# Optimization experiments

Measured on AMD Instinct MI355X. Metric: run time of the kernel, lower is better.

Reference implementation:

```python
import jax, jax.numpy as jnp
import numpy as np

N, E, B, D, R, L = 60000, 600000, 512, 128, 30, 3
CUT_LOW, CUT_HIGH = 0.0, 10.0
N_ATOM_TYPES = 100


def _sp(x, beta, threshold):
    # torch.nn.Softplus(beta, threshold): x if beta*x > threshold else log1p(exp(beta*x))/beta
    bx = beta * x
    return jnp.where(bx > threshold, x, jnp.log1p(jnp.exp(jnp.minimum(bx, threshold))) / beta)


def setup_inputs() -> dict:
    key = jax.random.key(0)
    ks = jax.random.split(key, 16)

    def lin(k, fi, fo):
        k1, k2 = jax.random.split(k)
        W = jax.random.normal(k1, (fi, fo), jnp.float32) * (fi ** -0.5)
        b = jax.random.normal(k2, (fo,), jnp.float32) * 0.01
        return W, b

    def lin_stack(k, fi, fo, n):
        Ws, bs = zip(*[lin(kk, fi, fo) for kk in jax.random.split(k, n)])
        return jnp.stack(Ws), jnp.stack(bs)

    inp = {}
    inp['atom_type'] = jax.random.randint(ks[0], (N,), 0, N_ATOM_TYPES)
    inp['src'] = jax.random.randint(ks[1], (E,), 0, N)
    inp['dst'] = jax.random.randint(ks[2], (E,), 0, N)
    inp['graph_ids'] = jnp.sort(jax.random.randint(ks[3], (N,), 0, B))
    inp['dist'] = jax.random.uniform(ks[4], (E,), jnp.float32) * CUT_HIGH
    inp['node_emb'] = jax.random.normal(ks[5], (N_ATOM_TYPES, D), jnp.float32) * 0.1
    inp['W_n1'], inp['b_n1'] = lin_stack(ks[6], D, D, L)
    inp['W_c1'], inp['b_c1'] = lin_stack(ks[7], R, D, L)
    inp['W_c2'], inp['b_c2'] = lin_stack(ks[8], D, D, L)
    inp['W_c3'], inp['b_c3'] = lin_stack(ks[9], D, D, L)
    inp['W_n2'], inp['b_n2'] = lin_stack(ks[10], D, D, L)
    inp['W_n3'], inp['b_n3'] = lin_stack(ks[11], D, D, L)
    inp['W_r1'], inp['b_r1'] = lin(ks[12], D * (L + 1), 64)
    inp['W_r2'], inp['b_r2'] = lin(ks[13], 64, 1)
    return inp


def reference(atom_type, src, dst, graph_ids, dist, node_emb,
              W_n1, b_n1, W_c1, b_c1, W_c2, b_c2, W_c3, b_c3,
              W_n2, b_n2, W_n3, b_n3, W_r1, b_r1, W_r2, b_r2):
    # RBF expansion of edge distances: exp(-(d - mu_k)^2 / gap)  -> [E, R]
    centers = jnp.linspace(CUT_LOW, CUT_HIGH, R).astype(dist.dtype)
    gap = centers[1] - centers[0]
    rbf = jnp.exp(-((dist[:, None] - centers) ** 2) / gap)

    h = node_emb[atom_type]  # node embedding lookup [N, D]
    hs = [h]
    for i in range(L):  # MultiLevelInteraction layers (fixed small count)
        h_new = hs[-1] @ W_n1[i] + b_n1[i]                       # node_layer1 [N, D]
        # VEConv edge MLP on rbf (linear1 -> softplus(0.5,14) -> linear2 -> linear3)
        e = _sp(rbf @ W_c1[i] + b_c1[i], 0.5, 14.0) @ W_c2[i] + b_c2[i]
        e = e @ W_c3[i] + b_c3[i]                                 # [E, D]
        # sum_e(h_new[src]*e) + sum_e(e) fused into one scatter-sum over dst
        msg = (h_new[src] + 1.0) * e                              # [E, D]
        node = jax.ops.segment_sum(msg, dst, num_segments=N)      # [N, D]
        new_node = _sp(node @ W_n2[i] + b_n2[i], 0.5, 14.0) @ W_n3[i] + b_n3[i]
        hs.append(hs[-1] + new_node)                              # residual h_i
    hcat = jnp.concatenate(hs, axis=1)                            # [N, D*(L+1)]
    out = _sp(hcat @ W_r1 + b_r1, 1.0, 20.0) @ W_r2 + b_r2        # [N, 1]
    # dgl.sum_nodes per molecule, then flatten -> [B]
    return jax.ops.segment_sum(out[:, 0], graph_ids, num_segments=B)
```

## Files before the change

### kernel.cpp

```cpp
#include <hip/hip_runtime.h>
#include <math.h>

#define N_NODES 60000
#define N_EDGES 600000
#define B_GRAPHS 512
#define DIM 128
#define RBF_R 30
#define NLAYERS 3
#define NBINS 1024
#define CHUNK 512
#define NCHUNK ((N_NODES + CHUNK - 1) / CHUNK)
#define NTILES (N_NODES / 16)

typedef __attribute__((ext_vector_type(8))) short bf16x8;
typedef __attribute__((ext_vector_type(4))) float f32x4;

__device__ __forceinline__ float sp05(float x) {
    float bx = 0.5f * x;
    return bx > 14.0f ? x : 2.0f * log1pf(expf(bx));
}
__device__ __forceinline__ float sp1(float x) {
    return x > 20.0f ? x : log1pf(expf(x));
}
__device__ __forceinline__ unsigned short f2bf(float f) {
    unsigned int u = __float_as_uint(f);
    unsigned int r = u + 0x7FFFu + ((u >> 16) & 1u);
    return (unsigned short)(r >> 16);
}
__device__ __forceinline__ float bf2f(unsigned int s) {
    return __uint_as_float(s << 16);
}

__device__ __forceinline__ size_t hidx(int row, int col) {
    return (size_t)((row >> 4) * 2048 + (col >> 5) * 512 +
                    ((((col >> 3) & 3) << 4) + (row & 15)) * 8 + (col & 7));
}

__global__ void k_conv(const float* __restrict__ Wn1, const float* __restrict__ Wn2,
                       const float* __restrict__ Wn3, const float* __restrict__ Wr1,
                       unsigned short* __restrict__ WtF, unsigned short* __restrict__ Wr1tF) {
    int i = blockIdx.x * 256 + threadIdx.x;
    if (i < 9 * 16384) {
        int mat = i >> 14, r = i & 16383;
        int frag = r >> 9, within = r & 511;
        int ks = frag >> 3, ntile = frag & 7;
        int lane = within >> 3, j = within & 7;
        int q = lane >> 4, l16 = lane & 15;
        int n = ntile * 16 + l16;
        int k = ks * 32 + q * 8 + j;
        const float* src = (mat < 3) ? (Wn1 + (size_t)mat * 16384)
                         : (mat < 6) ? (Wn2 + (size_t)(mat - 3) * 16384)
                                     : (Wn3 + (size_t)(mat - 6) * 16384);
        WtF[i] = f2bf(src[k * 128 + n]);
    } else {
        int ii = i - 9 * 16384;
        if (ii < 32768) {
            int frag = ii >> 9, within = ii & 511;
            int lvl = frag >> 4, ks = (frag >> 2) & 3, ntile = frag & 3;
            int lane = within >> 3, j = within & 7;
            int q = lane >> 4, l16 = lane & 15;
            int n = ntile * 16 + l16;
            int k = lvl * 128 + ks * 32 + q * 8 + j;
            Wr1tF[ii] = f2bf(Wr1[k * 64 + n]);
        }
    }
}

__global__ void k_embed(const int* __restrict__ atom_type,
                        const float* __restrict__ node_emb,
                        unsigned short* __restrict__ hb0) {
    int i = blockIdx.x * 256 + threadIdx.x;
    if (i >= N_NODES * DIM) return;
    int tile = i >> 11;
    int rem = i & 2047;
    int ks = rem >> 9;
    int lane = (rem >> 3) & 63;
    int j = rem & 7;
    int row = tile * 16 + (lane & 15);
    int col = ks * 32 + (lane >> 4) * 8 + j;
    hb0[i] = f2bf(node_emb[atom_type[row] * DIM + col]);
}


__global__ void k_hist(const int* __restrict__ dst, int* __restrict__ counts) {
    int e = blockIdx.x * blockDim.x + threadIdx.x;
    if (e >= N_EDGES) return;
    atomicAdd(&counts[dst[e]], 1);
}

__global__ void k_bsum(const int* __restrict__ counts, int* __restrict__ bsums) {
    __shared__ int red[256];
    int c = blockIdx.x, tid = threadIdx.x;
    int base = c * CHUNK;
    int v = 0;
    for (int i = tid; i < CHUNK; i += 256)
        if (base + i < N_NODES) v += counts[base + i];
    red[tid] = v;
    __syncthreads();
    for (int s = 128; s > 0; s >>= 1) {
        if (tid < s) red[tid] += red[tid + s];
        __syncthreads();
    }
    if (tid == 0) bsums[c] = red[0];
}

__global__ void k_scan_b(int* __restrict__ bsums) {
    __shared__ int sb[NCHUNK];
    int tid = threadIdx.x;
    if (tid < NCHUNK) sb[tid] = bsums[tid];
    __syncthreads();
    if (tid == 0) {
        int run = 0;
        for (int i = 0; i < NCHUNK; ++i) { int v = sb[i]; sb[i] = run; run += v; }
    }
    __syncthreads();
    if (tid < NCHUNK) bsums[tid] = sb[tid];
}

__global__ void k_scan_final(const int* __restrict__ counts, const int* __restrict__ bsums,
                             int* __restrict__ offsets) {
    __shared__ int sc[CHUNK];
    int c = blockIdx.x, tid = threadIdx.x;
    int base = c * CHUNK;
    for (int i = tid; i < CHUNK; i += 256)
        sc[i] = (base + i < N_NODES) ? counts[base + i] : 0;
    __syncthreads();
    if (tid == 0) {
        int run = bsums[c];
        for (int i = 0; i < CHUNK; ++i) { int v = sc[i]; sc[i] = run; run += v; }
    }
    __syncthreads();
    for (int i = tid; i < CHUNK; i += 256)
        if (base + i < N_NODES) offsets[base + i] = sc[i];
    if (c == 0 && tid == 0) offsets[N_NODES] = N_EDGES;
}

__global__ void k_fill(const int* __restrict__ src, const int* __restrict__ dst,
                       const float* __restrict__ dist,
                       const int* __restrict__ offsets, int* __restrict__ cnt2,
                       uint2* __restrict__ meta) {
    int e = blockIdx.x * blockDim.x + threadIdx.x;
    if (e >= N_EDGES) return;
    int d = dst[e];
    int pos = offsets[d] + atomicAdd(&cnt2[d], 1);
    float x = dist[e];
    float p = x * ((float)NBINS / 10.0f);
    int bin = (int)p;
    if (bin > NBINS - 1) bin = NBINS - 1;
    float w = p - (float)bin;
    int wq = (int)(w * 65535.0f + 0.5f);
    if (wq > 65535) wq = 65535;
    meta[pos] = make_uint2((unsigned)src[e], ((unsigned)bin << 16) | (unsigned)wq);
}


__global__ void k_table_all(const float* __restrict__ Wc1, const float* __restrict__ bc1,
                            const float* __restrict__ Wc2, const float* __restrict__ bc2,
                            const float* __restrict__ Wc3, const float* __restrict__ bc3,
                            unsigned short* __restrict__ tableb) {
    __shared__ float t[DIM];
    __shared__ float u[DIM];
    int lyr = blockIdx.x / (NBINS + 1);
    int b = blockIdx.x % (NBINS + 1);
    int d = threadIdx.x;
    const float* wc1 = Wc1 + (size_t)lyr * RBF_R * DIM;
    const float* wc2 = Wc2 + (size_t)lyr * DIM * DIM;
    const float* wc3 = Wc3 + (size_t)lyr * DIM * DIM;
    float dist = (float)b * (10.0f / (float)NBINS);
    const float gap = 10.0f / 29.0f;
    float acc = bc1[lyr * DIM + d];
#pragma unroll
    for (int k = 0; k < RBF_R; ++k) {
        float c = (float)k * (10.0f / 29.0f);
        float df = dist - c;
        acc += expf(-df * df / gap) * wc1[k * DIM + d];
    }
    t[d] = sp05(acc);
    __syncthreads();
    acc = bc2[lyr * DIM + d];
#pragma unroll 8
    for (int k = 0; k < DIM; ++k) acc += t[k] * wc2[k * DIM + d];
    u[d] = acc;
    __syncthreads();
    acc = bc3[lyr * DIM + d];
#pragma unroll 8
    for (int k = 0; k < DIM; ++k) acc += u[k] * wc3[k * DIM + d];
    tableb[((size_t)lyr * (NBINS + 1) + b) * DIM + d] = f2bf(acc);
}

__global__ void k_pack_all(const unsigned short* __restrict__ tableb,
                           unsigned int* __restrict__ packed) {
    int i = blockIdx.x * 256 + threadIdx.x;
    int lyr = i / (NBINS * DIM);
    int r = i % (NBINS * DIM);
    const unsigned short* tb = tableb + (size_t)lyr * (NBINS + 1) * DIM;
    float a = bf2f(tb[r]);
    float b = bf2f(tb[r + DIM]);
    packed[i] = (unsigned int)f2bf(a) | ((unsigned int)f2bf(b - a) << 16);
}


__global__ __launch_bounds__(256) void k_gemm_g(const unsigned short* __restrict__ Ab,
                                                const unsigned short* __restrict__ WtF,
                                                const float* __restrict__ bias,
                                                unsigned short* __restrict__ Cb) {
    int tid = threadIdx.x;
    int wave = tid >> 6, lane = tid & 63;
    int q = lane >> 4, l16 = lane & 15;
    int mhalf = wave & 1, nhalf = wave >> 1;
    int rb = blockIdx.x * 64 + mhalf * 32;
    int c0 = nhalf * 64;
    bf16x8 bfrag[4][4];
#pragma unroll
    for (int ks = 0; ks < 4; ++ks)
#pragma unroll
        for (int nt = 0; nt < 4; ++nt)
            bfrag[ks][nt] = *(const bf16x8*)&WtF[(size_t)(ks * 8 + nhalf * 4 + nt) * 512 + lane * 8];
    f32x4 acc[2][4] = {};
#pragma unroll
    for (int ks = 0; ks < 4; ++ks)
#pragma unroll
        for (int mt = 0; mt < 2; ++mt) {
            int tt = (rb >> 4) + mt;
            if (tt > NTILES - 1) tt = NTILES - 1;
            bf16x8 a = *(const bf16x8*)&Ab[(size_t)tt * 2048 + ks * 512 + lane * 8];
#pragma unroll
            for (int nt = 0; nt < 4; ++nt)
                acc[mt][nt] = __builtin_amdgcn_mfma_f32_16x16x32_bf16(a, bfrag[ks][nt], acc[mt][nt], 0, 0, 0);
        }
#pragma unroll
    for (int mt = 0; mt < 2; ++mt)
#pragma unroll
        for (int nt = 0; nt < 4; ++nt) {
            int col = c0 + nt * 16 + l16;
            float b = bias[col] + 1.0f;
#pragma unroll
            for (int r = 0; r < 4; ++r) {
                int row = rb + mt * 16 + q * 4 + r;
                if (row < N_NODES) Cb[(size_t)row * 128 + col] = f2bf(acc[mt][nt][r] + b);
            }
        }
}

__global__ __launch_bounds__(256) void k_gather(
    const int* __restrict__ offsets, const uint2* __restrict__ meta,
    const unsigned int* __restrict__ packed, const unsigned short* __restrict__ gb,
    unsigned short* __restrict__ nodeb) {
    int wave = threadIdx.x >> 6, lane = threadIdx.x & 63;
    int n = blockIdx.x * 4 + wave;
    int beg = offsets[n], end = offsets[n + 1];
    int off = lane * 2;
    const float ws = 1.0f / 65535.0f;
    float acc0 = 0.f, acc1 = 0.f, acc2 = 0.f, acc3 = 0.f;
    int j = beg;
    for (; j + 4 <= end; j += 4) {
        uint2 m0 = meta[j], m1 = meta[j + 1], m2 = meta[j + 2], m3 = meta[j + 3];
        uint2 p0 = *(const uint2*)&packed[(size_t)(m0.y >> 16) * DIM + off];
        uint2 p1 = *(const uint2*)&packed[(size_t)(m1.y >> 16) * DIM + off];
        uint2 p2 = *(const uint2*)&packed[(size_t)(m2.y >> 16) * DIM + off];
        uint2 p3 = *(const uint2*)&packed[(size_t)(m3.y >> 16) * DIM + off];
        unsigned int g0 = *(const unsigned int*)&gb[(size_t)m0.x * DIM + off];
        unsigned int g1 = *(const unsigned int*)&gb[(size_t)m1.x * DIM + off];
        unsigned int g2 = *(const unsigned int*)&gb[(size_t)m2.x * DIM + off];
        unsigned int g3 = *(const unsigned int*)&gb[(size_t)m3.x * DIM + off];
        float w0 = (float)(m0.y & 0xffff) * ws;
        float w1 = (float)(m1.y & 0xffff) * ws;
        float w2 = (float)(m2.y & 0xffff) * ws;
        float w3 = (float)(m3.y & 0xffff) * ws;
        acc0 += bf2f(g0 & 0xffff) * (bf2f(p0.x & 0xffff) + w0 * bf2f(p0.x >> 16));
        acc1 += bf2f(g0 >> 16)    * (bf2f(p0.y & 0xffff) + w0 * bf2f(p0.y >> 16));
        acc2 += bf2f(g1 & 0xffff) * (bf2f(p1.x & 0xffff) + w1 * bf2f(p1.x >> 16));
        acc3 += bf2f(g1 >> 16)    * (bf2f(p1.y & 0xffff) + w1 * bf2f(p1.y >> 16));
        acc0 += bf2f(g2 & 0xffff) * (bf2f(p2.x & 0xffff) + w2 * bf2f(p2.x >> 16));
        acc1 += bf2f(g2 >> 16)    * (bf2f(p2.y & 0xffff) + w2 * bf2f(p2.y >> 16));
        acc2 += bf2f(g3 & 0xffff) * (bf2f(p3.x & 0xffff) + w3 * bf2f(p3.x >> 16));
        acc3 += bf2f(g3 >> 16)    * (bf2f(p3.y & 0xffff) + w3 * bf2f(p3.y >> 16));
    }
    for (; j < end; ++j) {
        uint2 m0 = meta[j];
        uint2 p0 = *(const uint2*)&packed[(size_t)(m0.y >> 16) * DIM + off];
        unsigned int g0 = *(const unsigned int*)&gb[(size_t)m0.x * DIM + off];
        float w0 = (float)(m0.y & 0xffff) * ws;
        acc0 += bf2f(g0 & 0xffff) * (bf2f(p0.x & 0xffff) + w0 * bf2f(p0.x >> 16));
        acc1 += bf2f(g0 >> 16)    * (bf2f(p0.y & 0xffff) + w0 * bf2f(p0.y >> 16));
    }
    acc0 += acc2; acc1 += acc3;
    unsigned int o = (unsigned int)f2bf(acc0) | ((unsigned int)f2bf(acc1) << 16);
    *(unsigned int*)&nodeb[(size_t)n * DIM + off] = o;
}

__global__ __launch_bounds__(256) void k_node_update(
    const unsigned short* __restrict__ nodeb,
    const unsigned short* __restrict__ W2tF, const float* __restrict__ b2,
    const unsigned short* __restrict__ W3tF, const float* __restrict__ b3,
    const unsigned short* __restrict__ hb_in, unsigned short* __restrict__ hb_out,
    const unsigned short* __restrict__ WgF, const float* __restrict__ bg,
    unsigned short* __restrict__ gb, int do_g) {
    __shared__ unsigned short ts[64][136];
    __shared__ unsigned short hs[64][136];
    int tid = threadIdx.x;
    int wave = tid >> 6, lane = tid & 63;
    int q = lane >> 4, l16 = lane & 15;
    int mhalf = wave & 1, nhalf = wave >> 1;
    int rb = blockIdx.x * 64 + mhalf * 32;
    int c0 = nhalf * 64;

    bf16x8 bfrag[4][4];
#pragma unroll
    for (int ks = 0; ks < 4; ++ks)
#pragma unroll
        for (int nt = 0; nt < 4; ++nt)
            bfrag[ks][nt] = *(const bf16x8*)&W2tF[(size_t)(ks * 8 + nhalf * 4 + nt) * 512 + lane * 8];
    f32x4 acc[2][4] = {};
#pragma unroll
    for (int ks = 0; ks < 4; ++ks)
#pragma unroll
        for (int mt = 0; mt < 2; ++mt) {
            int m = rb + mt * 16 + l16;
            if (m > N_NODES - 1) m = N_NODES - 1;
            bf16x8 a = *(const bf16x8*)&nodeb[(size_t)m * 128 + ks * 32 + q * 8];
#pragma unroll
            for (int nt = 0; nt < 4; ++nt)
                acc[mt][nt] = __builtin_amdgcn_mfma_f32_16x16x32_bf16(a, bfrag[ks][nt], acc[mt][nt], 0, 0, 0);
        }
#pragma unroll
    for (int mt = 0; mt < 2; ++mt)
#pragma unroll
        for (int nt = 0; nt < 4; ++nt) {
            int col = c0 + nt * 16 + l16;
            float b = b2[col];
#pragma unroll
            for (int r = 0; r < 4; ++r) {
                int lrow = mhalf * 32 + mt * 16 + q * 4 + r;
                ts[lrow][col] = f2bf(sp05(acc[mt][nt][r] + b));
            }
        }
    __syncthreads();
#pragma unroll
    for (int ks = 0; ks < 4; ++ks)
#pragma unroll
        for (int nt = 0; nt < 4; ++nt)
            bfrag[ks][nt] = *(const bf16x8*)&W3tF[(size_t)(ks * 8 + nhalf * 4 + nt) * 512 + lane * 8];
#pragma unroll
    for (int mt = 0; mt < 2; ++mt)
#pragma unroll
        for (int nt = 0; nt < 4; ++nt) acc[mt][nt] = (f32x4){0.f, 0.f, 0.f, 0.f};
#pragma unroll
    for (int ks = 0; ks < 4; ++ks)
#pragma unroll
        for (int mt = 0; mt < 2; ++mt) {
            int lrow = mhalf * 32 + mt * 16 + l16;
            bf16x8 a = *(const bf16x8*)&ts[lrow][ks * 32 + q * 8];
#pragma unroll
            for (int nt = 0; nt < 4; ++nt)
                acc[mt][nt] = __builtin_amdgcn_mfma_f32_16x16x32_bf16(a, bfrag[ks][nt], acc[mt][nt], 0, 0, 0);
        }
#pragma unroll
    for (int mt = 0; mt < 2; ++mt)
#pragma unroll
        for (int nt = 0; nt < 4; ++nt) {
            int col = c0 + nt * 16 + l16;
            float b = b3[col];
#pragma unroll
            for (int r = 0; r < 4; ++r) {
                int row = rb + mt * 16 + q * 4 + r;
                int lrow = mhalf * 32 + mt * 16 + q * 4 + r;
                if (row < N_NODES) {
                    size_t idx = hidx(row, col);
                    float v = bf2f(hb_in[idx]) + acc[mt][nt][r] + b;
                    unsigned short bf = f2bf(v);
                    hb_out[idx] = bf;
                    hs[lrow][col] = bf;
                } else {
                    hs[lrow][col] = 0;
                }
            }
        }
    if (!do_g) return;
    __syncthreads();
#pragma unroll
    for (int ks = 0; ks < 4; ++ks)
#pragma unroll
        for (int nt = 0; nt < 4; ++nt)
            bfrag[ks][nt] = *(const bf16x8*)&WgF[(size_t)(ks * 8 + nhalf * 4 + nt) * 512 + lane * 8];
#pragma unroll
    for (int mt = 0; mt < 2; ++mt)
#pragma unroll
        for (int nt = 0; nt < 4; ++nt) acc[mt][nt] = (f32x4){0.f, 0.f, 0.f, 0.f};
#pragma unroll
    for (int ks = 0; ks < 4; ++ks)
#pragma unroll
        for (int mt = 0; mt < 2; ++mt) {
            int lrow = mhalf * 32 + mt * 16 + l16;
            bf16x8 a = *(const bf16x8*)&hs[lrow][ks * 32 + q * 8];
#pragma unroll
            for (int nt = 0; nt < 4; ++nt)
                acc[mt][nt] = __builtin_amdgcn_mfma_f32_16x16x32_bf16(a, bfrag[ks][nt], acc[mt][nt], 0, 0, 0);
        }
#pragma unroll
    for (int mt = 0; mt < 2; ++mt)
#pragma unroll
        for (int nt = 0; nt < 4; ++nt) {
            int col = c0 + nt * 16 + l16;
            float b = bg[col] + 1.0f;
#pragma unroll
            for (int r = 0; r < 4; ++r) {
                int row = rb + mt * 16 + q * 4 + r;
                if (row < N_NODES) gb[(size_t)row * 128 + col] = f2bf(acc[mt][nt][r] + b);
            }
        }
}

__global__ __launch_bounds__(256) void k_readout(
    const unsigned short* __restrict__ hb0, const unsigned short* __restrict__ hb1,
    const unsigned short* __restrict__ hb2, const unsigned short* __restrict__ hb3,
    const unsigned short* __restrict__ Wr1tF, const float* __restrict__ br1,
    const float* __restrict__ Wr2, const float* __restrict__ br2,
    const int* __restrict__ graph_ids, float* __restrict__ out) {
    int tid = threadIdx.x;
    int wave = tid >> 6, lane = tid & 63;
    int q = lane >> 4, l16 = lane & 15;
    int rb0 = blockIdx.x * 128 + wave * 16;
    const unsigned short* hbs[4] = {hb0, hb1, hb2, hb3};
    f32x4 acc[2][4] = {};
    for (int lvl = 0; lvl < 4; ++lvl) {
        bf16x8 bfrag[4][4];
#pragma unroll
        for (int ks = 0; ks < 4; ++ks)
#pragma unroll
            for (int nt = 0; nt < 4; ++nt)
                bfrag[ks][nt] = *(const bf16x8*)&Wr1tF[(size_t)((lvl * 4 + ks) * 4 + nt) * 512 + lane * 8];
        const unsigned short* Ab = hbs[lvl];
#pragma unroll
        for (int ks = 0; ks < 4; ++ks)
#pragma unroll
            for (int mt = 0; mt < 2; ++mt) {
                int tt = blockIdx.x * 8 + wave + mt * 4;
                if (tt > NTILES - 1) tt = NTILES - 1;
                bf16x8 a = *(const bf16x8*)&Ab[(size_t)tt * 2048 + ks * 512 + lane * 8];
#pragma unroll
                for (int nt = 0; nt < 4; ++nt)
                    acc[mt][nt] = __builtin_amdgcn_mfma_f32_16x16x32_bf16(a, bfrag[ks][nt], acc[mt][nt], 0, 0, 0);
            }
    }
    float brr = br2[0];
#pragma unroll
    for (int mt = 0; mt < 2; ++mt) {
        float partial[4] = {0.f, 0.f, 0.f, 0.f};
#pragma unroll
        for (int nt = 0; nt < 4; ++nt) {
            int col = nt * 16 + l16;
            float b = br1[col];
            float w = Wr2[col];
#pragma unroll
            for (int r = 0; r < 4; ++r) partial[r] += sp1(acc[mt][nt][r] + b) * w;
        }
#pragma unroll
        for (int r = 0; r < 4; ++r) {
            float v = partial[r];
            v += __shfl_xor(v, 1); v += __shfl_xor(v, 2);
            v += __shfl_xor(v, 4); v += __shfl_xor(v, 8);
            if (l16 == 0) {
                int row = rb0 + mt * 64 + q * 4 + r;
                if (row < N_NODES) atomicAdd(&out[graph_ids[row]], v + brr);
            }
        }
    }
}

extern "C" void kernel_launch(void* const* d_in, const int* in_sizes, int n_in,
                              void* d_out, int out_size, void* d_ws, size_t ws_size,
                              hipStream_t stream) {
    const int* atom_type   = (const int*)d_in[0];
    const int* src         = (const int*)d_in[1];
    const int* dst         = (const int*)d_in[2];
    const int* graph_ids   = (const int*)d_in[3];
    const float* dist      = (const float*)d_in[4];
    const float* node_emb  = (const float*)d_in[5];
    const float* W_n1 = (const float*)d_in[6];  const float* b_n1 = (const float*)d_in[7];
    const float* W_c1 = (const float*)d_in[8];  const float* b_c1 = (const float*)d_in[9];
    const float* W_c2 = (const float*)d_in[10]; const float* b_c2 = (const float*)d_in[11];
    const float* W_c3 = (const float*)d_in[12]; const float* b_c3 = (const float*)d_in[13];
    const float* W_n2 = (const float*)d_in[14]; const float* b_n2 = (const float*)d_in[15];
    const float* W_n3 = (const float*)d_in[16]; const float* b_n3 = (const float*)d_in[17];
    const float* W_r1 = (const float*)d_in[18]; const float* b_r1 = (const float*)d_in[19];
    const float* W_r2 = (const float*)d_in[20]; const float* b_r2 = (const float*)d_in[21];
    float* out = (float*)d_out;

    size_t ND = (size_t)N_NODES * DIM;
    uint2* meta   = (uint2*)d_ws;
    int* offsets  = (int*)(meta + N_EDGES);
    int* counts   = offsets + 60008;
    int* cnt2     = counts + N_NODES;
    int* bsums    = cnt2 + N_NODES;
    unsigned int* packed = (unsigned int*)(bsums + 128);
    unsigned short* hb0    = (unsigned short*)(packed + (size_t)3 * NBINS * DIM);
    unsigned short* hb1    = hb0 + ND;
    unsigned short* hb2    = hb1 + ND;
    unsigned short* hb3    = hb2 + ND;
    unsigned short* gb     = hb3 + ND;
    unsigned short* nodeb  = gb + ND;
    unsigned short* tableb = nodeb + ND;
    unsigned short* WtF    = tableb + (size_t)3 * (NBINS + 1) * DIM;
    unsigned short* Wr1tF  = WtF + 9 * 16384;

    unsigned short* hbp[4] = {hb0, hb1, hb2, hb3};

    hipMemsetAsync(out, 0, B_GRAPHS * sizeof(float), stream);
    hipMemsetAsync(counts, 0, (2 * N_NODES + 128) * sizeof(int), stream);

    k_conv<<<(9 * 16384 + 32768 + 255) / 256, 256, 0, stream>>>(
        W_n1, W_n2, W_n3, W_r1, WtF, Wr1tF);
    k_embed<<<(N_NODES * DIM) / 256, 256, 0, stream>>>(atom_type, node_emb, hb0);
    k_table_all<<<3 * (NBINS + 1), DIM, 0, stream>>>(
        W_c1, b_c1, W_c2, b_c2, W_c3, b_c3, tableb);
    k_pack_all<<<(3 * NBINS * DIM) / 256, 256, 0, stream>>>(tableb, packed);

    k_hist<<<(N_EDGES + 255) / 256, 256, 0, stream>>>(dst, counts);
    k_bsum<<<NCHUNK, 256, 0, stream>>>(counts, bsums);
    k_scan_b<<<1, 128, 0, stream>>>(bsums);
    k_scan_final<<<NCHUNK, 256, 0, stream>>>(counts, bsums, offsets);
    k_fill<<<(N_EDGES + 255) / 256, 256, 0, stream>>>(src, dst, dist, offsets, cnt2, meta);

    int gblocks = (N_NODES + 63) / 64;
    int rblocks = (N_NODES + 127) / 128;
    k_gemm_g<<<gblocks, 256, 0, stream>>>(hb0, WtF, b_n1, gb);
    for (int i = 0; i < NLAYERS; ++i) {
        k_gather<<<N_NODES / 4, 256, 0, stream>>>(
            offsets, meta, packed + (size_t)i * NBINS * DIM, gb, nodeb);
        int do_g = (i < NLAYERS - 1) ? 1 : 0;
        k_node_update<<<gblocks, 256, 0, stream>>>(
            nodeb, WtF + (size_t)(3 + i) * 16384, b_n2 + (size_t)i * DIM,
            WtF + (size_t)(6 + i) * 16384, b_n3 + (size_t)i * DIM,
            hbp[i], hbp[i + 1],
            WtF + (size_t)(i + 1) * 16384, b_n1 + (size_t)(i + 1 < 3 ? i + 1 : 0) * DIM,
            gb, do_g);
    }
    k_readout<<<rblocks, 256, 0, stream>>>(
        hb0, hb1, hb2, hb3, Wr1tF, b_r1, W_r2, b_r2, graph_ids, out);
}
```

Before: 569.9 us.

## Merge setup kernels into one launch and preload readout activations

Four setup kernels (weight conversion, embedding lookup, edge-table MLP, table packing) are folded into one kernel that dispatches on block index. The table blocks now compute two adjacent bins per block, so the packed base/delta table is written directly with no intermediate table buffer. The readout kernel loads all activation fragments for the four levels up front and uses launch_bounds(256,1), trading register pressure and occupancy for fewer launches and better load overlap. The table path now recomputes each bin roughly twice, and the shared-memory branch inside a mixed-role kernel may raise resource use for every block.

```diff
diff --git a/kernel.cpp b/kernel.cpp
--- a/kernel.cpp
+++ b/kernel.cpp
@@ -12,6 +12,10 @@
 #define NCHUNK ((N_NODES + CHUNK - 1) / CHUNK)
 #define NTILES (N_NODES / 16)
 
+#define NB_CONV 704
+#define NB_EMBED 30000
+#define NB_TABLE (3 * NBINS)
+
 typedef __attribute__((ext_vector_type(8))) short bf16x8;
 typedef __attribute__((ext_vector_type(4))) float f32x4;
 
@@ -36,25 +40,33 @@
                     ((((col >> 3) & 3) << 4) + (row & 15)) * 8 + (col & 7));
 }
 
-__global__ void k_conv(const float* __restrict__ Wn1, const float* __restrict__ Wn2,
-                       const float* __restrict__ Wn3, const float* __restrict__ Wr1,
-                       unsigned short* __restrict__ WtF, unsigned short* __restrict__ Wr1tF) {
-    int i = blockIdx.x * 256 + threadIdx.x;
-    if (i < 9 * 16384) {
-        int mat = i >> 14, r = i & 16383;
-        int frag = r >> 9, within = r & 511;
-        int ks = frag >> 3, ntile = frag & 7;
-        int lane = within >> 3, j = within & 7;
-        int q = lane >> 4, l16 = lane & 15;
-        int n = ntile * 16 + l16;
-        int k = ks * 32 + q * 8 + j;
-        const float* src = (mat < 3) ? (Wn1 + (size_t)mat * 16384)
-                         : (mat < 6) ? (Wn2 + (size_t)(mat - 3) * 16384)
-                                     : (Wn3 + (size_t)(mat - 6) * 16384);
-        WtF[i] = f2bf(src[k * 128 + n]);
-    } else {
-        int ii = i - 9 * 16384;
-        if (ii < 32768) {
+__global__ __launch_bounds__(256) void k_setup(
+    const float* __restrict__ Wn1, const float* __restrict__ Wn2,
+    const float* __restrict__ Wn3, const float* __restrict__ Wr1,
+    const int* __restrict__ atom_type, const float* __restrict__ node_emb,
+    const float* __restrict__ Wc1, const float* __restrict__ bc1,
+    const float* __restrict__ Wc2, const float* __restrict__ bc2,
+    const float* __restrict__ Wc3, const float* __restrict__ bc3,
+    unsigned short* __restrict__ WtF, unsigned short* __restrict__ Wr1tF,
+    unsigned short* __restrict__ hb0, unsigned int* __restrict__ packed) {
+    int b = blockIdx.x;
+    int tid = threadIdx.x;
+    if (b < NB_CONV) {
+        int i = b * 256 + tid;
+        if (i < 9 * 16384) {
+            int mat = i >> 14, r = i & 16383;
+            int frag = r >> 9, within = r & 511;
+            int ks = frag >> 3, ntile = frag & 7;
+            int lane = within >> 3, j = within & 7;
+            int q = lane >> 4, l16 = lane & 15;
+            int n = ntile * 16 + l16;
+            int k = ks * 32 + q * 8 + j;
+            const float* src = (mat < 3) ? (Wn1 + (size_t)mat * 16384)
+                             : (mat < 6) ? (Wn2 + (size_t)(mat - 3) * 16384)
+                                         : (Wn3 + (size_t)(mat - 6) * 16384);
+            WtF[i] = f2bf(src[k * 128 + n]);
+        } else {
+            int ii = i - 9 * 16384;
             int frag = ii >> 9, within = ii & 511;
             int lvl = frag >> 4, ks = (frag >> 2) & 3, ntile = frag & 3;
             int lane = within >> 3, j = within & 7;
@@ -63,22 +75,60 @@
             int k = lvl * 128 + ks * 32 + q * 8 + j;
             Wr1tF[ii] = f2bf(Wr1[k * 64 + n]);
         }
-    }
-}
-
-__global__ void k_embed(const int* __restrict__ atom_type,
-                        const float* __restrict__ node_emb,
-                        unsigned short* __restrict__ hb0) {
-    int i = blockIdx.x * 256 + threadIdx.x;
-    if (i >= N_NODES * DIM) return;
-    int tile = i >> 11;
-    int rem = i & 2047;
-    int ks = rem >> 9;
-    int lane = (rem >> 3) & 63;
-    int j = rem & 7;
-    int row = tile * 16 + (lane & 15);
-    int col = ks * 32 + (lane >> 4) * 8 + j;
-    hb0[i] = f2bf(node_emb[atom_type[row] * DIM + col]);
+        return;
+    }
+    if (b < NB_CONV + NB_EMBED) {
+        int i = (b - NB_CONV) * 256 + tid;
+        int tile = i >> 11;
+        int rem = i & 2047;
+        int ks = rem >> 9;
+        int lane = (rem >> 3) & 63;
+        int j = rem & 7;
+        int row = tile * 16 + (lane & 15);
+        int col = ks * 32 + (lane >> 4) * 8 + j;
+        hb0[i] = f2bf(node_emb[atom_type[row] * DIM + col]);
+        return;
+    }
+    {
+        __shared__ float t[2][DIM];
+        __shared__ float u[2][DIM];
+        __shared__ float va[2][DIM];
+        int idx = b - NB_CONV - NB_EMBED;
+        int lyr = idx / NBINS;
+        int bin = idx % NBINS;
+        int half = tid >> 7;
+        int d = tid & 127;
+        const float* wc1 = Wc1 + (size_t)lyr * RBF_R * DIM;
+        const float* wc2 = Wc2 + (size_t)lyr * DIM * DIM;
+        const float* wc3 = Wc3 + (size_t)lyr * DIM * DIM;
+        float dist = (float)(bin + half) * (10.0f / (float)NBINS);
+        const float gap = 10.0f / 29.0f;
+        float acc = bc1[lyr * DIM + d];
+#pragma unroll
+        for (int k = 0; k < RBF_R; ++k) {
+            float c = (float)k * (10.0f / 29.0f);
+            float df = dist - c;
+            acc += expf(-df * df / gap) * wc1[k * DIM + d];
+        }
+        t[half][d] = sp05(acc);
+        __syncthreads();
+        acc = bc2[lyr * DIM + d];
+#pragma unroll 8
+        for (int k = 0; k < DIM; ++k) acc += t[half][k] * wc2[k * DIM + d];
+        u[half][d] = acc;
+        __syncthreads();
+        acc = bc3[lyr * DIM + d];
+#pragma unroll 8
+        for (int k = 0; k < DIM; ++k) acc += u[half][k] * wc3[k * DIM + d];
+        va[half][d] = acc;
+        __syncthreads();
+        if (half == 0) {
+            float a = bf2f(f2bf(va[0][d]));
+            float bv = bf2f(f2bf(va[1][d]));
+            packed[((size_t)lyr * NBINS + bin) * DIM + d] =
+                (unsigned int)f2bf(a) | ((unsigned int)f2bf(bv - a) << 16);
+        }
+    }
 }
 
 
@@ -151,52 +201,6 @@
     int wq = (int)(w * 65535.0f + 0.5f);
     if (wq > 65535) wq = 65535;
     meta[pos] = make_uint2((unsigned)src[e], ((unsigned)bin << 16) | (unsigned)wq);
-}
-
-
-__global__ void k_table_all(const float* __restrict__ Wc1, const float* __restrict__ bc1,
-                            const float* __restrict__ Wc2, const float* __restrict__ bc2,
-                            const float* __restrict__ Wc3, const float* __restrict__ bc3,
-                            unsigned short* __restrict__ tableb) {
-    __shared__ float t[DIM];
-    __shared__ float u[DIM];
-    int lyr = blockIdx.x / (NBINS + 1);
-    int b = blockIdx.x % (NBINS + 1);
-    int d = threadIdx.x;
-    const float* wc1 = Wc1 + (size_t)lyr * RBF_R * DIM;
-    const float* wc2 = Wc2 + (size_t)lyr * DIM * DIM;
-    const float* wc3 = Wc3 + (size_t)lyr * DIM * DIM;
-    float dist = (float)b * (10.0f / (float)NBINS);
-    const float gap = 10.0f / 29.0f;
-    float acc = bc1[lyr * DIM + d];
-#pragma unroll
-    for (int k = 0; k < RBF_R; ++k) {
-        float c = (float)k * (10.0f / 29.0f);
-        float df = dist - c;
-        acc += expf(-df * df / gap) * wc1[k * DIM + d];
-    }
-    t[d] = sp05(acc);
-    __syncthreads();
-    acc = bc2[lyr * DIM + d];
-#pragma unroll 8
-    for (int k = 0; k < DIM; ++k) acc += t[k] * wc2[k * DIM + d];
-    u[d] = acc;
-    __syncthreads();
-    acc = bc3[lyr * DIM + d];
-#pragma unroll 8
-    for (int k = 0; k < DIM; ++k) acc += u[k] * wc3[k * DIM + d];
-    tableb[((size_t)lyr * (NBINS + 1) + b) * DIM + d] = f2bf(acc);
-}
-
-__global__ void k_pack_all(const unsigned short* __restrict__ tableb,
-                           unsigned int* __restrict__ packed) {
-    int i = blockIdx.x * 256 + threadIdx.x;
-    int lyr = i / (NBINS * DIM);
-    int r = i % (NBINS * DIM);
-    const unsigned short* tb = tableb + (size_t)lyr * (NBINS + 1) * DIM;
-    float a = bf2f(tb[r]);
-    float b = bf2f(tb[r + DIM]);
-    packed[i] = (unsigned int)f2bf(a) | ((unsigned int)f2bf(b - a) << 16);
 }
 
 
@@ -411,7 +415,7 @@
         }
 }
 
-__global__ __launch_bounds__(256) void k_readout(
+__global__ __launch_bounds__(256, 1) void k_readout(
     const unsigned short* __restrict__ hb0, const unsigned short* __restrict__ hb1,
     const unsigned short* __restrict__ hb2, const unsigned short* __restrict__ hb3,
     const unsigned short* __restrict__ Wr1tF, const float* __restrict__ br1,
@@ -421,8 +425,24 @@
     int wave = tid >> 6, lane = tid & 63;
     int q = lane >> 4, l16 = lane & 15;
     int rb0 = blockIdx.x * 128 + wave * 16;
+    int tt0 = blockIdx.x * 8 + wave;
+    int tt1 = tt0 + 4;
+    if (tt0 > NTILES - 1) tt0 = NTILES - 1;
+    if (tt1 > NTILES - 1) tt1 = NTILES - 1;
+
+    bf16x8 a[4][2][4];
     const unsigned short* hbs[4] = {hb0, hb1, hb2, hb3};
+#pragma unroll
+    for (int lvl = 0; lvl < 4; ++lvl) {
+        const unsigned short* Ab = hbs[lvl];
+#pragma unroll
+        for (int ks = 0; ks < 4; ++ks) {
+            a[lvl][0][ks] = *(const bf16x8*)&Ab[(size_t)tt0 * 2048 + ks * 512 + lane * 8];
+            a[lvl][1][ks] = *(const bf16x8*)&Ab[(size_t)tt1 * 2048 + ks * 512 + lane * 8];
+        }
+    }
     f32x4 acc[2][4] = {};
+#pragma unroll
     for (int lvl = 0; lvl < 4; ++lvl) {
         bf16x8 bfrag[4][4];
 #pragma unroll
@@ -430,18 +450,13 @@
 #pragma unroll
             for (int nt = 0; nt < 4; ++nt)
                 bfrag[ks][nt] = *(const bf16x8*)&Wr1tF[(size_t)((lvl * 4 + ks) * 4 + nt) * 512 + lane * 8];
-        const unsigned short* Ab = hbs[lvl];
 #pragma unroll
         for (int ks = 0; ks < 4; ++ks)
 #pragma unroll
-            for (int mt = 0; mt < 2; ++mt) {
-                int tt = blockIdx.x * 8 + wave + mt * 4;
-                if (tt > NTILES - 1) tt = NTILES - 1;
-                bf16x8 a = *(const bf16x8*)&Ab[(size_t)tt * 2048 + ks * 512 + lane * 8];
+            for (int mt = 0; mt < 2; ++mt)
 #pragma unroll
                 for (int nt = 0; nt < 4; ++nt)
-                    acc[mt][nt] = __builtin_amdgcn_mfma_f32_16x16x32_bf16(a, bfrag[ks][nt], acc[mt][nt], 0, 0, 0);
-            }
+                    acc[mt][nt] = __builtin_amdgcn_mfma_f32_16x16x32_bf16(a[lvl][mt][ks], bfrag[ks][nt], acc[mt][nt], 0, 0, 0);
     }
     float brr = br2[0];
 #pragma unroll
@@ -500,8 +515,7 @@
     unsigned short* hb3    = hb2 + ND;
     unsigned short* gb     = hb3 + ND;
     unsigned short* nodeb  = gb + ND;
-    unsigned short* tableb = nodeb + ND;
-    unsigned short* WtF    = tableb + (size_t)3 * (NBINS + 1) * DIM;
+    unsigned short* WtF    = nodeb + ND;
     unsigned short* Wr1tF  = WtF + 9 * 16384;
 
     unsigned short* hbp[4] = {hb0, hb1, hb2, hb3};
@@ -509,12 +523,10 @@
     hipMemsetAsync(out, 0, B_GRAPHS * sizeof(float), stream);
     hipMemsetAsync(counts, 0, (2 * N_NODES + 128) * sizeof(int), stream);
 
-    k_conv<<<(9 * 16384 + 32768 + 255) / 256, 256, 0, stream>>>(
-        W_n1, W_n2, W_n3, W_r1, WtF, Wr1tF);
-    k_embed<<<(N_NODES * DIM) / 256, 256, 0, stream>>>(atom_type, node_emb, hb0);
-    k_table_all<<<3 * (NBINS + 1), DIM, 0, stream>>>(
-        W_c1, b_c1, W_c2, b_c2, W_c3, b_c3, tableb);
-    k_pack_all<<<(3 * NBINS * DIM) / 256, 256, 0, stream>>>(tableb, packed);
+    k_setup<<<NB_CONV + NB_EMBED + NB_TABLE, 256, 0, stream>>>(
+        W_n1, W_n2, W_n3, W_r1, atom_type, node_emb,
+        W_c1, b_c1, W_c2, b_c2, W_c3, b_c3,
+        WtF, Wr1tF, hb0, packed);
 
     k_hist<<<(N_EDGES + 255) / 256, 256, 0, stream>>>(dst, counts);
     k_bsum<<<NCHUNK, 256, 0, stream>>>(counts, bsums);
```

After: 575.4 us. Within noise of the previous version (+1.0%).
